# Optimization experiments

Hardware: AMD Instinct MI355X
Metric: run time of the kernel (lower is better)

Reference implementation:

```python
import jax, jax.numpy as jnp
import numpy as np
import math

B, N, FIN, FOUT, OPE = 16, 2048, 128, 128, 64


def setup_inputs() -> dict:
    key = jax.random.key(0)
    ks = jax.random.split(key, 10)
    h = jax.random.normal(ks[0], (B, N, FIN), dtype=jnp.float32)
    adj = jax.random.randint(ks[1], (B, N, N), 0, 2).astype(jnp.float32)
    op_emb = jax.random.normal(ks[2], (B, N, OPE), dtype=jnp.float32)
    # Linear weights stored as (in, out) so y = x @ W; torch init scale ~ 1/sqrt(fan_in)
    s_in = 1.0 / math.sqrt(FIN)
    Wk = jax.random.uniform(ks[3], (FIN, FOUT), minval=-s_in, maxval=s_in)
    Wq = jax.random.uniform(ks[4], (FIN, FOUT), minval=-s_in, maxval=s_in)
    Wv = jax.random.uniform(ks[5], (FIN, FOUT), minval=-s_in, maxval=s_in)
    s_a = 1.0 / math.sqrt(FOUT)
    a_w = jax.random.uniform(ks[6], (FOUT,), minval=-s_a, maxval=s_a)
    s_op = 1.0 / math.sqrt(OPE)
    op_W = jax.random.uniform(ks[7], (OPE, FOUT), minval=-s_op, maxval=s_op)
    op_b = jax.random.uniform(ks[8], (FOUT,), minval=-s_op, maxval=s_op)
    ln_g = jnp.ones((FOUT,), dtype=jnp.float32)
    ln_b = jnp.zeros((FOUT,), dtype=jnp.float32)
    return {"h": h, "adj": adj, "op_emb": op_emb, "Wk": Wk, "Wq": Wq,
            "Wv": Wv, "a_w": a_w, "op_W": op_W, "op_b": op_b,
            "ln_g": ln_g, "ln_b": ln_b}


def reference(h, adj, op_emb, Wk, Wq, Wv, a_w, op_W, op_b, ln_g, ln_b):
    d = Wk.shape[1]
    Whk = h @ Wk  # (B,N,d)
    Whq = h @ Wq
    Whv = h @ Wv
    # Original builds a_input[b,e,l,m] = Whq[b,e,m]*Whk[b,l,m] (B,N,N,d) then
    # projects with a (d->1). Algebraically: scores[b,e,l] = <Whq[b,e], Whk[b,l]*a_w>.
    scores = jnp.einsum('bed,bld->bel', Whq, Whk * a_w)
    scores = scores / jnp.sqrt(jnp.float32(d))  # attention_rescale
    alpha = jax.nn.leaky_relu(scores, negative_slope=0.2)  # leakrelu
    alpha = alpha * adj  # multiplicative mask (zeros stay in the softmax)
    attn = jax.nn.softmax(alpha, axis=-1)  # softmax over source nodes l
    agg = jnp.einsum('bel,bld->bed', attn, Whv)  # (B,N,d)
    gate = jax.nn.sigmoid(op_emb @ op_W + op_b)  # opattention branch
    hp = gate * agg
    # LayerNorm over last dim, eps=1e-5
    mu = jnp.mean(hp, axis=-1, keepdims=True)
    var = jnp.mean(jnp.square(hp - mu), axis=-1, keepdims=True)
    return (hp - mu) * jax.lax.rsqrt(var + 1e-5) * ln_g + ln_b
```

## Files before the change

### kernel.cpp

```cpp
#include <hip/hip_runtime.h>
#include <hip/hip_bf16.h>

typedef unsigned int u32;
typedef unsigned long long u64;
typedef float f32x4 __attribute__((ext_vector_type(4)));
typedef short s16x8 __attribute__((ext_vector_type(8)));

#define LDA 136

#define WQT_OFF 0ULL
#define WKT_OFF 32768ULL
#define WVT_OFF 65536ULL
#define OPWT_OFF 98304ULL
#define Q_OFF 114688ULL
#define K_OFF (Q_OFF + 8388608ULL)
#define VT_OFF (K_OFF + 8388608ULL)
#define GATE_OFF (VT_OFF + 8388608ULL)

__device__ __forceinline__ u32 f2bf(float f) {
  u32 u = __float_as_uint(f);
  return (u + 0x7fffu + ((u >> 16) & 1u)) >> 16;
}

__device__ __forceinline__ u32 pk2bf(float a, float b) {
  __hip_bfloat162 h = __float22bfloat162_rn(make_float2(a, b));
  u32 r;
  __builtin_memcpy(&r, &h, 4);
  return r;
}

__device__ __forceinline__ void gl_lds16(const void* g, void* l) {
  __builtin_amdgcn_global_load_lds((const __attribute__((address_space(1))) void*)g,
                                   (__attribute__((address_space(3))) void*)l, 16, 0, 0);
}

__global__ void k0_wt(const float* Wq, const float* Wk, const float* Wv,
                      const float* aw, const float* opW, char* ws) {
  int nt = blockIdx.x, part = blockIdx.y;
  int kksh = (nt == 3) ? 6 : 7;
  int KK = 1 << kksh;
  const float* S = (nt == 0) ? Wq : (nt == 1) ? Wk : (nt == 2) ? Wv : opW;
  unsigned short* D = (unsigned short*)(ws + (nt == 0 ? WQT_OFF : nt == 1 ? WKT_OFF : nt == 2 ? WVT_OFF : OPWT_OFF));
  int base = part * 8 * KK;
  for (int i = threadIdx.x; i < 8 * KK; i += 256) {
    int d = part * 8 + (i >> kksh), k = i & (KK - 1);
    float v = S[k * 128 + d];
    if (nt == 1) v *= aw[d] * 0.12751743f;
    D[base + i] = (unsigned short)f2bf(v);
  }
}

__launch_bounds__(256, 2)
__global__ void k1_proj(const float* __restrict__ h, const float* __restrict__ op_emb,
                        const float* __restrict__ op_b, char* __restrict__ ws) {
  int nt = blockIdx.x, et = blockIdx.y;
  int kksh = (nt == 3) ? 6 : 7;
  int KK = 1 << kksh;
  __shared__ unsigned short bufA[128 * LDA];
  __shared__ unsigned short bufB[128 * LDA];
  unsigned short* wbuf = (nt == 2) ? bufB : bufA;
  unsigned short* xbuf = (nt == 2) ? bufA : bufB;
  const unsigned short* Wt = (const unsigned short*)(ws + (nt == 0 ? WQT_OFF : nt == 1 ? WKT_OFF : nt == 2 ? WVT_OFF : OPWT_OFF));
  {
    const uint4* Ws = (const uint4*)Wt;
    int cnt = 128 * KK / 8;
    for (int i = threadIdx.x; i < cnt; i += 256) {
      uint4 v = Ws[i];
      int r = (8 * i) >> kksh, c = (8 * i) & (KK - 1);
      *(uint4*)&wbuf[r * LDA + c] = v;
    }
  }
  {
    const float* X = (nt == 3) ? (op_emb + (size_t)et * 128 * 64) : (h + (size_t)et * 128 * 128);
    int cnt = 128 * KK / 4;
    for (int i = threadIdx.x; i < cnt; i += 256) {
      float4 v = *(const float4*)(X + 4 * i);
      int r = (4 * i) >> kksh, c = (4 * i) & (KK - 1);
      *(uint2*)&xbuf[r * LDA + c] = make_uint2(pk2bf(v.x, v.y), pk2bf(v.z, v.w));
    }
  }
  __syncthreads();
  int tid = threadIdx.x, w = tid >> 6, lane = tid & 63, l15 = lane & 15, q = lane >> 4;
  int wa = w >> 1, wb = w & 1;
  f32x4 acc[4][4];
#pragma unroll
  for (int a = 0; a < 4; a++)
#pragma unroll
    for (int bq = 0; bq < 4; bq++) acc[a][bq] = f32x4{0.f, 0.f, 0.f, 0.f};
  for (int ks = 0; ks < KK / 32; ks++) {
    s16x8 af[4], bf_[4];
#pragma unroll
    for (int mt = 0; mt < 4; mt++)
      af[mt] = *(const s16x8*)&bufA[(wa * 64 + mt * 16 + l15) * LDA + ks * 32 + q * 8];
#pragma unroll
    for (int n2 = 0; n2 < 4; n2++)
      bf_[n2] = *(const s16x8*)&bufB[(wb * 64 + n2 * 16 + l15) * LDA + ks * 32 + q * 8];
#pragma unroll
    for (int mt = 0; mt < 4; mt++)
#pragma unroll
      for (int n2 = 0; n2 < 4; n2++)
        acc[mt][n2] = __builtin_amdgcn_mfma_f32_16x16x32_bf16(af[mt], bf_[n2], acc[mt][n2], 0, 0, 0);
  }
  if (nt <= 1) {
    unsigned short* Dst = (unsigned short*)(ws + (nt == 0 ? Q_OFF : K_OFF));
#pragma unroll
    for (int mt = 0; mt < 4; mt++)
#pragma unroll
      for (int n2 = 0; n2 < 4; n2++) {
        int d0 = wa * 64 + mt * 16 + q * 4;
        int eg = et * 128 + wb * 64 + n2 * 16 + l15;
        f32x4 a = acc[mt][n2];
        *(uint2*)(Dst + (size_t)eg * 128 + d0) = make_uint2(pk2bf(a[0], a[1]), pk2bf(a[2], a[3]));
      }
  } else if (nt == 2) {
    unsigned short* Dst = (unsigned short*)(ws + VT_OFF);
    int b = et >> 4;
    int ein0 = (et & 15) * 128;
#pragma unroll
    for (int mt = 0; mt < 4; mt++)
#pragma unroll
      for (int n2 = 0; n2 < 4; n2++) {
        int e0b = ein0 + wa * 64 + mt * 16 + q * 4;
        int d = wb * 64 + n2 * 16 + l15;
        f32x4 a = acc[mt][n2];
        *(uint2*)(Dst + (size_t)b * 128 * 2048 + (size_t)d * 2048 + e0b) =
            make_uint2(pk2bf(a[0], a[1]), pk2bf(a[2], a[3]));
      }
  } else {
    float* Dst = (float*)(ws + GATE_OFF);
#pragma unroll
    for (int mt = 0; mt < 4; mt++)
#pragma unroll
      for (int n2 = 0; n2 < 4; n2++) {
        int d0 = wa * 64 + mt * 16 + q * 4;
        int eg = et * 128 + wb * 64 + n2 * 16 + l15;
        f32x4 a = acc[mt][n2];
        float4 g4;
        g4.x = 1.f / (1.f + __builtin_amdgcn_exp2f(-(a[0] + op_b[d0 + 0]) * 1.4426950f));
        g4.y = 1.f / (1.f + __builtin_amdgcn_exp2f(-(a[1] + op_b[d0 + 1]) * 1.4426950f));
        g4.z = 1.f / (1.f + __builtin_amdgcn_exp2f(-(a[2] + op_b[d0 + 2]) * 1.4426950f));
        g4.w = 1.f / (1.f + __builtin_amdgcn_exp2f(-(a[3] + op_b[d0 + 3]) * 1.4426950f));
        *(float4*)(Dst + (size_t)eg * 128 + d0) = g4;
      }
  }
}

#define BAR_A do { asm volatile("s_waitcnt vmcnt(8) lgkmcnt(0)\n\ts_barrier" ::: "memory"); \
                   __builtin_amdgcn_sched_barrier(0); } while (0)
#define BAR_B do { asm volatile("s_waitcnt vmcnt(0) lgkmcnt(0)\n\ts_barrier" ::: "memory"); \
                   __builtin_amdgcn_sched_barrier(0); } while (0)
#define BAR_C do { asm volatile("s_waitcnt lgkmcnt(0)\n\ts_barrier" ::: "memory"); \
                   __builtin_amdgcn_sched_barrier(0); } while (0)

__launch_bounds__(256, 2)
__global__ void k2_attn(const float* __restrict__ adj, const float* __restrict__ ln_g,
                        const float* __restrict__ ln_b, char* __restrict__ ws,
                        float* __restrict__ out) {
  __shared__ char smem[81920];
  char* Klds = smem;
  char* Vlds = smem + 32768;
  char* PL = smem + 65536;

  const int bid = blockIdx.x;
  const int xcd = bid & 7, slot = bid >> 3;
  const int b = xcd * 2 + (slot >> 5);
  const int e0 = (slot & 31) << 6;

  const unsigned short* Qg = (const unsigned short*)(ws + Q_OFF) + ((size_t)b * 2048 + e0) * 128;
  const unsigned short* Kg = (const unsigned short*)(ws + K_OFF) + (size_t)b * 2048 * 128;
  const unsigned short* Vtg = (const unsigned short*)(ws + VT_OFF) + (size_t)b * 128 * 2048;
  const float* gateg = (const float*)(ws + GATE_OFF) + ((size_t)b * 2048 + e0) * 128;
  const float* adjg = adj + (size_t)b * 2048 * 2048 + (size_t)e0 * 2048;

  const int tid = threadIdx.x;
  const int w = tid >> 6, lane = tid & 63, l15 = lane & 15, q = lane >> 4;
  const int wh = w >> 1, we = w & 1;

  s16x8 qf[2][4];
#pragma unroll
  for (int et = 0; et < 2; et++) {
    const int e = we * 32 + et * 16 + l15;
#pragma unroll
    for (int ks = 0; ks < 4; ks++)
      qf[et][ks] = *(const s16x8*)(Qg + (size_t)e * 128 + ks * 32 + q * 8);
  }
  __builtin_amdgcn_sched_barrier(0);

  f32x4 oacc[2][4];
#pragma unroll
  for (int et = 0; et < 2; et++)
#pragma unroll
    for (int dt = 0; dt < 4; dt++) oacc[et][dt] = f32x4{0.f, 0.f, 0.f, 0.f};
  float dp0 = 0.0f, dp1 = 0.0f;
  float4 av[2][4];

#pragma unroll
  for (int j = 0; j < 8; j++) {
    int S = (j * 4 + w) * 64 + lane;
    int r = S >> 4, c = (S & 15) ^ (r & 15);
    gl_lds16(Kg + (size_t)r * 128 + (c << 3), Klds + (j * 4 + w) * 1024);
  }
  __builtin_amdgcn_sched_barrier(0);
#pragma unroll
  for (int j = 0; j < 8; j++) {
    int S = (j * 4 + w) * 64 + lane;
    int r = S >> 4, c = (S & 15) ^ (r & 15);
    gl_lds16(Vtg + (size_t)r * 2048 + (c << 3), Vlds + (j * 4 + w) * 1024);
  }
  __builtin_amdgcn_sched_barrier(0);
#pragma unroll
  for (int et = 0; et < 2; et++) {
    const int e = we * 32 + et * 16 + l15;
#pragma unroll
    for (int lt = 0; lt < 4; lt++)
      av[et][lt] = *(const float4*)(adjg + (size_t)e * 2048 + wh * 64 + lt * 16 + q * 4);
  }
  __builtin_amdgcn_sched_barrier(0);

#pragma unroll 1
  for (int it = 0; it < 16; it++) {
    BAR_A;

    f32x4 sacc[4][2];
#pragma unroll
    for (int lt = 0; lt < 4; lt++)
#pragma unroll
      for (int et = 0; et < 2; et++) sacc[lt][et] = f32x4{0.f, 0.f, 0.f, 0.f};
#pragma unroll
    for (int ks = 0; ks < 4; ks++) {
      s16x8 kf[4];
#pragma unroll
      for (int lt = 0; lt < 4; lt++) {
        int l = wh * 64 + lt * 16 + l15;
        kf[lt] = *(const s16x8*)(Klds + l * 256 + (((ks * 4 + q) ^ l15) << 4));
      }
#pragma unroll
      for (int lt = 0; lt < 4; lt++)
#pragma unroll
        for (int et = 0; et < 2; et++)
          sacc[lt][et] = __builtin_amdgcn_mfma_f32_16x16x32_bf16(kf[lt], qf[et][ks], sacc[lt][et], 0, 0, 0);
    }

#pragma unroll
    for (int et = 0; et < 2; et++) {
      const int e = we * 32 + et * 16 + l15;
      float dsum = 0.0f;
#pragma unroll
      for (int lt = 0; lt < 4; lt++) {
        float4 aj = av[et][lt];
        f32x4 s = sacc[lt][et];
        float p0 = __builtin_amdgcn_exp2f(fmaxf(s[0], 0.2f * s[0]) * aj.x);
        float p1 = __builtin_amdgcn_exp2f(fmaxf(s[1], 0.2f * s[1]) * aj.y);
        float p2 = __builtin_amdgcn_exp2f(fmaxf(s[2], 0.2f * s[2]) * aj.z);
        float p3 = __builtin_amdgcn_exp2f(fmaxf(s[3], 0.2f * s[3]) * aj.w);
        dsum += (p0 + p1) + (p2 + p3);
        int chunk = wh * 8 + lt * 2 + (q >> 1);
        *(uint2*)(PL + e * 256 + ((chunk ^ l15) << 4) + (q & 1) * 8) =
            make_uint2(pk2bf(p0, p1), pk2bf(p2, p3));
      }
      if (et == 0) dp0 += dsum; else dp1 += dsum;
    }

    BAR_B;

    if (it < 15) {
      const unsigned short* kb = Kg + (size_t)(it + 1) * 16384;
#pragma unroll
      for (int j = 0; j < 8; j++) {
        int S = (j * 4 + w) * 64 + lane;
        int r = S >> 4, c = (S & 15) ^ (r & 15);
        gl_lds16(kb + (size_t)r * 128 + (c << 3), Klds + (j * 4 + w) * 1024);
      }
      __builtin_amdgcn_sched_barrier(0);
      const float* ab = adjg + (size_t)(it + 1) * 128;
#pragma unroll
      for (int et = 0; et < 2; et++) {
        const int e = we * 32 + et * 16 + l15;
#pragma unroll
        for (int lt = 0; lt < 4; lt++)
          av[et][lt] = *(const float4*)(ab + (size_t)e * 2048 + wh * 64 + lt * 16 + q * 4);
      }
      __builtin_amdgcn_sched_barrier(0);
    }

#pragma unroll
    for (int ks = 0; ks < 4; ks++) {
      s16x8 af[2], vf[4];
#pragma unroll
      for (int et = 0; et < 2; et++) {
        const int e = we * 32 + et * 16 + l15;
        af[et] = *(const s16x8*)(PL + e * 256 + (((ks * 4 + q) ^ l15) << 4));
      }
#pragma unroll
      for (int dt = 0; dt < 4; dt++) {
        int d = wh * 64 + dt * 16 + l15;
        vf[dt] = *(const s16x8*)(Vlds + d * 256 + (((ks * 4 + q) ^ l15) << 4));
      }
#pragma unroll
      for (int et = 0; et < 2; et++)
#pragma unroll
        for (int dt = 0; dt < 4; dt++)
          oacc[et][dt] = __builtin_amdgcn_mfma_f32_16x16x32_bf16(af[et], vf[dt], oacc[et][dt], 0, 0, 0);
    }

    BAR_C;

    if (it < 15) {
      const unsigned short* vb = Vtg + (size_t)(it + 1) * 128;
#pragma unroll
      for (int j = 0; j < 8; j++) {
        int S = (j * 4 + w) * 64 + lane;
        int r = S >> 4, c = (S & 15) ^ (r & 15);
        gl_lds16(vb + (size_t)r * 2048 + (c << 3), Vlds + (j * 4 + w) * 1024);
      }
      __builtin_amdgcn_sched_barrier(0);
    }
  }

  float* sden = (float*)(smem + 65536);
  if (tid < 64) sden[tid] = 0.0f;
  __syncthreads();
  atomicAdd(&sden[we * 32 + l15], dp0);
  atomicAdd(&sden[we * 32 + 16 + l15], dp1);

  float* O2 = (float*)smem;
#pragma unroll
  for (int et = 0; et < 2; et++)
#pragma unroll
    for (int dt = 0; dt < 4; dt++) {
      const int eb = we * 32 + et * 16 + q * 4;
      const int d = wh * 64 + dt * 16 + l15;
      f32x4 v = oacc[et][dt];
#pragma unroll
      for (int r = 0; r < 4; r++) O2[(eb + r) * 132 + d] = v[r];
    }
  __syncthreads();

  {
    const int e = tid >> 2, j = tid & 3;
    const float inv = 1.0f / sden[e];
    const float* row = O2 + e * 132 + j * 32;
    const float* gr = gateg + (size_t)e * 128 + j * 32;
    float4 x[8];
    float s1 = 0.f, s2 = 0.f;
#pragma unroll
    for (int i = 0; i < 8; i++) {
      float4 v = *(const float4*)(row + i * 4);
      float4 g = *(const float4*)(gr + i * 4);
      float4 hp;
      hp.x = v.x * inv * g.x; hp.y = v.y * inv * g.y;
      hp.z = v.z * inv * g.z; hp.w = v.w * inv * g.w;
      x[i] = hp;
      s1 += (hp.x + hp.y) + (hp.z + hp.w);
      s2 += (hp.x * hp.x + hp.y * hp.y) + (hp.z * hp.z + hp.w * hp.w);
    }
    s1 += __shfl_xor(s1, 1); s2 += __shfl_xor(s2, 1);
    s1 += __shfl_xor(s1, 2); s2 += __shfl_xor(s2, 2);
    const float mu = s1 * 0.0078125f;
    const float var = s2 * 0.0078125f - mu * mu;
    const float rs = rsqrtf(var + 1e-5f);
    float* orow = out + ((size_t)b * 2048 + e0 + e) * 128 + j * 32;
    const float* gg = ln_g + j * 32;
    const float* bb = ln_b + j * 32;
#pragma unroll
    for (int i = 0; i < 8; i++) {
      float4 gv = *(const float4*)(gg + i * 4);
      float4 bv = *(const float4*)(bb + i * 4);
      float4 o;
      o.x = (x[i].x - mu) * rs * gv.x + bv.x;
      o.y = (x[i].y - mu) * rs * gv.y + bv.y;
      o.z = (x[i].z - mu) * rs * gv.z + bv.z;
      o.w = (x[i].w - mu) * rs * gv.w + bv.w;
      *(float4*)(orow + i * 4) = o;
    }
  }
}

extern "C" void kernel_launch(void* const* d_in, const int* in_sizes, int n_in,
                              void* d_out, int out_size, void* d_ws, size_t ws_size,
                              hipStream_t stream) {
  const float* h = (const float*)d_in[0];
  const float* adj = (const float*)d_in[1];
  const float* op_emb = (const float*)d_in[2];
  const float* Wk = (const float*)d_in[3];
  const float* Wq = (const float*)d_in[4];
  const float* Wv = (const float*)d_in[5];
  const float* a_w = (const float*)d_in[6];
  const float* op_W = (const float*)d_in[7];
  const float* op_b = (const float*)d_in[8];
  const float* ln_g = (const float*)d_in[9];
  const float* ln_b = (const float*)d_in[10];
  char* ws = (char*)d_ws;
  float* out = (float*)d_out;

  k0_wt<<<dim3(4, 16), 256, 0, stream>>>(Wq, Wk, Wv, a_w, op_W, ws);
  k1_proj<<<dim3(4, 256), 256, 0, stream>>>(h, op_emb, op_b, ws);
  k2_attn<<<512, 256, 0, stream>>>(adj, ln_g, ln_b, ws, out);
}
```

Before: 449.1 us.

## Double-buffer adjacency registers to prefetch two iterations ahead in attention loop

The main attention loop is unrolled by two so that adjacency tiles for iteration it+2 are loaded into alternating register sets (avA/avB) while the current iteration computes. The vmcnt waits are adjusted so that K/V loads into LDS are awaited without draining the outstanding adj loads. This hides global-load latency for the adj mask, which is the largest HBM stream. In exchange it uses more VGPRs, which could hurt occupancy at the two-blocks-per-CU launch bound, and the hand-counted vmcnt values must match the issue order exactly.

Measured after the change: 553.6 us. +23.3%, slower.

```diff
diff --git a/kernel.cpp b/kernel.cpp
--- a/kernel.cpp
+++ b/kernel.cpp
@@ -2,7 +2,6 @@
 #include <hip/hip_bf16.h>
 
 typedef unsigned int u32;
-typedef unsigned long long u64;
 typedef float f32x4 __attribute__((ext_vector_type(4)));
 typedef short s16x8 __attribute__((ext_vector_type(8)));
 
@@ -145,12 +144,119 @@
   }
 }
 
-#define BAR_A do { asm volatile("s_waitcnt vmcnt(8) lgkmcnt(0)\n\ts_barrier" ::: "memory"); \
-                   __builtin_amdgcn_sched_barrier(0); } while (0)
-#define BAR_B do { asm volatile("s_waitcnt vmcnt(0) lgkmcnt(0)\n\ts_barrier" ::: "memory"); \
-                   __builtin_amdgcn_sched_barrier(0); } while (0)
-#define BAR_C do { asm volatile("s_waitcnt lgkmcnt(0)\n\ts_barrier" ::: "memory"); \
-                   __builtin_amdgcn_sched_barrier(0); } while (0)
+
+#define BAR_A16 do { asm volatile("s_waitcnt vmcnt(16) lgkmcnt(0)\n\ts_barrier" ::: "memory"); \
+                     __builtin_amdgcn_sched_barrier(0); } while (0)
+#define BAR_A8  do { asm volatile("s_waitcnt vmcnt(8) lgkmcnt(0)\n\ts_barrier" ::: "memory"); \
+                     __builtin_amdgcn_sched_barrier(0); } while (0)
+#define BAR_B8  do { asm volatile("s_waitcnt vmcnt(8) lgkmcnt(0)\n\ts_barrier" ::: "memory"); \
+                     __builtin_amdgcn_sched_barrier(0); } while (0)
+#define BAR_B0  do { asm volatile("s_waitcnt vmcnt(0) lgkmcnt(0)\n\ts_barrier" ::: "memory"); \
+                     __builtin_amdgcn_sched_barrier(0); } while (0)
+#define BAR_C   do { asm volatile("s_waitcnt lgkmcnt(0)\n\ts_barrier" ::: "memory"); \
+                     __builtin_amdgcn_sched_barrier(0); } while (0)
+
+#define ISSUE_K(ITP1) do { \
+  const unsigned short* kb_ = Kg + (size_t)(ITP1) * 16384; \
+  _Pragma("unroll") \
+  for (int j_ = 0; j_ < 8; j_++) { \
+    int S_ = (j_ * 4 + w) * 64 + lane; \
+    int r_ = S_ >> 4, c_ = (S_ & 15) ^ (r_ & 15); \
+    gl_lds16(kb_ + (size_t)r_ * 128 + (c_ << 3), Klds + (j_ * 4 + w) * 1024); \
+  } \
+  __builtin_amdgcn_sched_barrier(0); \
+} while (0)
+
+#define ISSUE_V(ITP1) do { \
+  const unsigned short* vb_ = Vtg + (size_t)(ITP1) * 128; \
+  _Pragma("unroll") \
+  for (int j_ = 0; j_ < 8; j_++) { \
+    int S_ = (j_ * 4 + w) * 64 + lane; \
+    int r_ = S_ >> 4, c_ = (S_ & 15) ^ (r_ & 15); \
+    gl_lds16(vb_ + (size_t)r_ * 2048 + (c_ << 3), Vlds + (j_ * 4 + w) * 1024); \
+  } \
+  __builtin_amdgcn_sched_barrier(0); \
+} while (0)
+
+#define ISSUE_ADJ(ITN, AV) do { \
+  const float* ab_ = adjg + (size_t)(ITN) * 128; \
+  _Pragma("unroll") \
+  for (int et_ = 0; et_ < 2; et_++) { \
+    const int e_ = we * 32 + et_ * 16 + l15; \
+    _Pragma("unroll") \
+    for (int lt_ = 0; lt_ < 4; lt_++) \
+      AV[et_][lt_] = *(const float4*)(ab_ + (size_t)e_ * 2048 + wh * 64 + lt_ * 16 + q * 4); \
+  } \
+  __builtin_amdgcn_sched_barrier(0); \
+} while (0)
+
+#define K2_ITER(IT, AV, BARA, BARB, DO_ISS, DO_ADJ2) do { \
+  BARA;  \
+  f32x4 sacc[4][2]; \
+  _Pragma("unroll") \
+  for (int lt = 0; lt < 4; lt++) \
+    _Pragma("unroll") \
+    for (int et = 0; et < 2; et++) sacc[lt][et] = f32x4{0.f, 0.f, 0.f, 0.f}; \
+  _Pragma("unroll") \
+  for (int ks = 0; ks < 4; ks++) { \
+    s16x8 kf[4]; \
+    _Pragma("unroll") \
+    for (int lt = 0; lt < 4; lt++) { \
+      int l = wh * 64 + lt * 16 + l15; \
+      kf[lt] = *(const s16x8*)(Klds + l * 256 + (((ks * 4 + q) ^ l15) << 4)); \
+    } \
+    _Pragma("unroll") \
+    for (int lt = 0; lt < 4; lt++) \
+      _Pragma("unroll") \
+      for (int et = 0; et < 2; et++) \
+        sacc[lt][et] = __builtin_amdgcn_mfma_f32_16x16x32_bf16(kf[lt], qf[et][ks], sacc[lt][et], 0, 0, 0); \
+  } \
+  _Pragma("unroll") \
+  for (int et = 0; et < 2; et++) { \
+    const int e = we * 32 + et * 16 + l15; \
+    float dsum = 0.0f; \
+    _Pragma("unroll") \
+    for (int lt = 0; lt < 4; lt++) { \
+      float4 aj = AV[et][lt]; \
+      f32x4 s = sacc[lt][et]; \
+      float p0 = __builtin_amdgcn_exp2f(fmaxf(s[0], 0.2f * s[0]) * aj.x); \
+      float p1 = __builtin_amdgcn_exp2f(fmaxf(s[1], 0.2f * s[1]) * aj.y); \
+      float p2 = __builtin_amdgcn_exp2f(fmaxf(s[2], 0.2f * s[2]) * aj.z); \
+      float p3 = __builtin_amdgcn_exp2f(fmaxf(s[3], 0.2f * s[3]) * aj.w); \
+      dsum += (p0 + p1) + (p2 + p3); \
+      int chunk = wh * 8 + lt * 2 + (q >> 1); \
+      *(uint2*)(PL + e * 256 + ((chunk ^ l15) << 4) + (q & 1) * 8) = \
+          make_uint2(pk2bf(p0, p1), pk2bf(p2, p3)); \
+    } \
+    if (et == 0) dp0 += dsum; else dp1 += dsum; \
+  } \
+  BARB;  \
+  if (DO_ISS) ISSUE_K((IT) + 1); \
+  _Pragma("unroll") \
+  for (int ks = 0; ks < 4; ks++) { \
+    s16x8 af[2], vf[4]; \
+    _Pragma("unroll") \
+    for (int et = 0; et < 2; et++) { \
+      const int e = we * 32 + et * 16 + l15; \
+      af[et] = *(const s16x8*)(PL + e * 256 + (((ks * 4 + q) ^ l15) << 4)); \
+    } \
+    _Pragma("unroll") \
+    for (int dt = 0; dt < 4; dt++) { \
+      int d = wh * 64 + dt * 16 + l15; \
+      vf[dt] = *(const s16x8*)(Vlds + d * 256 + (((ks * 4 + q) ^ l15) << 4)); \
+    } \
+    _Pragma("unroll") \
+    for (int et = 0; et < 2; et++) \
+      _Pragma("unroll") \
+      for (int dt = 0; dt < 4; dt++) \
+        oacc[et][dt] = __builtin_amdgcn_mfma_f32_16x16x32_bf16(af[et], vf[dt], oacc[et][dt], 0, 0, 0); \
+  } \
+  BAR_C;  \
+  if (DO_ISS) { \
+    ISSUE_V((IT) + 1); \
+    if (DO_ADJ2) ISSUE_ADJ((IT) + 2, AV); \
+  } \
+} while (0)
 
 __launch_bounds__(256, 2)
 __global__ void k2_attn(const float* __restrict__ adj, const float* __restrict__ ln_g,
@@ -184,6 +290,7 @@
     for (int ks = 0; ks < 4; ks++)
       qf[et][ks] = *(const s16x8*)(Qg + (size_t)e * 128 + ks * 32 + q * 8);
   }
+  asm volatile("s_waitcnt vmcnt(0)" ::: "memory");
   __builtin_amdgcn_sched_barrier(0);
 
   f32x4 oacc[2][4];
@@ -192,130 +299,21 @@
 #pragma unroll
     for (int dt = 0; dt < 4; dt++) oacc[et][dt] = f32x4{0.f, 0.f, 0.f, 0.f};
   float dp0 = 0.0f, dp1 = 0.0f;
-  float4 av[2][4];
-
-#pragma unroll
-  for (int j = 0; j < 8; j++) {
-    int S = (j * 4 + w) * 64 + lane;
-    int r = S >> 4, c = (S & 15) ^ (r & 15);
-    gl_lds16(Kg + (size_t)r * 128 + (c << 3), Klds + (j * 4 + w) * 1024);
-  }
-  __builtin_amdgcn_sched_barrier(0);
-#pragma unroll
-  for (int j = 0; j < 8; j++) {
-    int S = (j * 4 + w) * 64 + lane;
-    int r = S >> 4, c = (S & 15) ^ (r & 15);
-    gl_lds16(Vtg + (size_t)r * 2048 + (c << 3), Vlds + (j * 4 + w) * 1024);
-  }
-  __builtin_amdgcn_sched_barrier(0);
-#pragma unroll
-  for (int et = 0; et < 2; et++) {
-    const int e = we * 32 + et * 16 + l15;
-#pragma unroll
-    for (int lt = 0; lt < 4; lt++)
-      av[et][lt] = *(const float4*)(adjg + (size_t)e * 2048 + wh * 64 + lt * 16 + q * 4);
-  }
-  __builtin_amdgcn_sched_barrier(0);
+  float4 avA[2][4], avB[2][4];
+
+  ISSUE_ADJ(0, avA);
+  ISSUE_K(0);
+  ISSUE_V(0);
+  ISSUE_ADJ(1, avB);
 
 #pragma unroll 1
-  for (int it = 0; it < 16; it++) {
-    BAR_A;
-
-    f32x4 sacc[4][2];
-#pragma unroll
-    for (int lt = 0; lt < 4; lt++)
-#pragma unroll
-      for (int et = 0; et < 2; et++) sacc[lt][et] = f32x4{0.f, 0.f, 0.f, 0.f};
-#pragma unroll
-    for (int ks = 0; ks < 4; ks++) {
-      s16x8 kf[4];
-#pragma unroll
-      for (int lt = 0; lt < 4; lt++) {
-        int l = wh * 64 + lt * 16 + l15;
-        kf[lt] = *(const s16x8*)(Klds + l * 256 + (((ks * 4 + q) ^ l15) << 4));
-      }
-#pragma unroll
-      for (int lt = 0; lt < 4; lt++)
-#pragma unroll
-        for (int et = 0; et < 2; et++)
-          sacc[lt][et] = __builtin_amdgcn_mfma_f32_16x16x32_bf16(kf[lt], qf[et][ks], sacc[lt][et], 0, 0, 0);
-    }
-
-#pragma unroll
-    for (int et = 0; et < 2; et++) {
-      const int e = we * 32 + et * 16 + l15;
-      float dsum = 0.0f;
-#pragma unroll
-      for (int lt = 0; lt < 4; lt++) {
-        float4 aj = av[et][lt];
-        f32x4 s = sacc[lt][et];
-        float p0 = __builtin_amdgcn_exp2f(fmaxf(s[0], 0.2f * s[0]) * aj.x);
-        float p1 = __builtin_amdgcn_exp2f(fmaxf(s[1], 0.2f * s[1]) * aj.y);
-        float p2 = __builtin_amdgcn_exp2f(fmaxf(s[2], 0.2f * s[2]) * aj.z);
-        float p3 = __builtin_amdgcn_exp2f(fmaxf(s[3], 0.2f * s[3]) * aj.w);
-        dsum += (p0 + p1) + (p2 + p3);
-        int chunk = wh * 8 + lt * 2 + (q >> 1);
-        *(uint2*)(PL + e * 256 + ((chunk ^ l15) << 4) + (q & 1) * 8) =
-            make_uint2(pk2bf(p0, p1), pk2bf(p2, p3));
-      }
-      if (et == 0) dp0 += dsum; else dp1 += dsum;
-    }
-
-    BAR_B;
-
-    if (it < 15) {
-      const unsigned short* kb = Kg + (size_t)(it + 1) * 16384;
-#pragma unroll
-      for (int j = 0; j < 8; j++) {
-        int S = (j * 4 + w) * 64 + lane;
-        int r = S >> 4, c = (S & 15) ^ (r & 15);
-        gl_lds16(kb + (size_t)r * 128 + (c << 3), Klds + (j * 4 + w) * 1024);
-      }
-      __builtin_amdgcn_sched_barrier(0);
-      const float* ab = adjg + (size_t)(it + 1) * 128;
-#pragma unroll
-      for (int et = 0; et < 2; et++) {
-        const int e = we * 32 + et * 16 + l15;
-#pragma unroll
-        for (int lt = 0; lt < 4; lt++)
-          av[et][lt] = *(const float4*)(ab + (size_t)e * 2048 + wh * 64 + lt * 16 + q * 4);
-      }
-      __builtin_amdgcn_sched_barrier(0);
-    }
-
-#pragma unroll
-    for (int ks = 0; ks < 4; ks++) {
-      s16x8 af[2], vf[4];
-#pragma unroll
-      for (int et = 0; et < 2; et++) {
-        const int e = we * 32 + et * 16 + l15;
-        af[et] = *(const s16x8*)(PL + e * 256 + (((ks * 4 + q) ^ l15) << 4));
-      }
-#pragma unroll
-      for (int dt = 0; dt < 4; dt++) {
-        int d = wh * 64 + dt * 16 + l15;
-        vf[dt] = *(const s16x8*)(Vlds + d * 256 + (((ks * 4 + q) ^ l15) << 4));
-      }
-#pragma unroll
-      for (int et = 0; et < 2; et++)
-#pragma unroll
-        for (int dt = 0; dt < 4; dt++)
-          oacc[et][dt] = __builtin_amdgcn_mfma_f32_16x16x32_bf16(af[et], vf[dt], oacc[et][dt], 0, 0, 0);
-    }
-
-    BAR_C;
-
-    if (it < 15) {
-      const unsigned short* vb = Vtg + (size_t)(it + 1) * 128;
-#pragma unroll
-      for (int j = 0; j < 8; j++) {
-        int S = (j * 4 + w) * 64 + lane;
-        int r = S >> 4, c = (S & 15) ^ (r & 15);
-        gl_lds16(vb + (size_t)r * 2048 + (c << 3), Vlds + (j * 4 + w) * 1024);
-      }
-      __builtin_amdgcn_sched_barrier(0);
-    }
-  }
+  for (int it2 = 0; it2 < 7; it2++) {
+    const int itE = it2 * 2;
+    K2_ITER(itE, avA, BAR_A16, BAR_B8, true, true);
+    K2_ITER(itE + 1, avB, BAR_A16, BAR_B8, true, true);
+  }
+  K2_ITER(14, avA, BAR_A16, BAR_B8, true, false);
+  K2_ITER(15, avB, BAR_A8, BAR_B0, false, false);
 
   float* sden = (float*)(smem + 65536);
   if (tid < 64) sden[tid] = 0.0f;
```

## Stage K/V tiles through registers instead of direct global-to-LDS loads

Applied to the files above, without the earlier changes.

Replaces the direct global_load_lds transfers of K and V tiles with ordinary global loads into registers at the top of each iteration, followed by register-to-LDS stores after the barriers. Offsets are precomputed once per thread. The aim is a register-prefetch pipeline: next-tile loads are issued early and overlap the score and PV MFMA work, and the vmcnt waits at the barriers go away. The cost is 16 extra uint4 registers per thread under launch bounds of 2 blocks per CU, which may cause spills or lower occupancy, plus extra VALU/LDS store instructions.

New measurement: 585.8 us. 1.3x slower.

```diff
diff --git a/kernel.cpp b/kernel.cpp
--- a/kernel.cpp
+++ b/kernel.cpp
@@ -2,7 +2,6 @@
 #include <hip/hip_bf16.h>
 
 typedef unsigned int u32;
-typedef unsigned long long u64;
 typedef float f32x4 __attribute__((ext_vector_type(4)));
 typedef short s16x8 __attribute__((ext_vector_type(8)));
 
@@ -27,11 +26,6 @@
   u32 r;
   __builtin_memcpy(&r, &h, 4);
   return r;
-}
-
-__device__ __forceinline__ void gl_lds16(const void* g, void* l) {
-  __builtin_amdgcn_global_load_lds((const __attribute__((address_space(1))) void*)g,
-                                   (__attribute__((address_space(3))) void*)l, 16, 0, 0);
 }
 
 __global__ void k0_wt(const float* Wq, const float* Wk, const float* Wv,
@@ -145,12 +139,8 @@
   }
 }
 
-#define BAR_A do { asm volatile("s_waitcnt vmcnt(8) lgkmcnt(0)\n\ts_barrier" ::: "memory"); \
-                   __builtin_amdgcn_sched_barrier(0); } while (0)
-#define BAR_B do { asm volatile("s_waitcnt vmcnt(0) lgkmcnt(0)\n\ts_barrier" ::: "memory"); \
-                   __builtin_amdgcn_sched_barrier(0); } while (0)
-#define BAR_C do { asm volatile("s_waitcnt lgkmcnt(0)\n\ts_barrier" ::: "memory"); \
-                   __builtin_amdgcn_sched_barrier(0); } while (0)
+#define BARL do { asm volatile("s_waitcnt lgkmcnt(0)\n\ts_barrier" ::: "memory"); \
+                  __builtin_amdgcn_sched_barrier(0); } while (0)
 
 __launch_bounds__(256, 2)
 __global__ void k2_attn(const float* __restrict__ adj, const float* __restrict__ ln_g,
@@ -176,6 +166,17 @@
   const int w = tid >> 6, lane = tid & 63, l15 = lane & 15, q = lane >> 4;
   const int wh = w >> 1, we = w & 1;
 
+  int ldsoff[8];
+  size_t koff[8], voff[8];
+#pragma unroll
+  for (int j = 0; j < 8; j++) {
+    int S = (j * 4 + w) * 64 + lane;
+    int r = S >> 4, c = (S & 15) ^ (r & 15);
+    ldsoff[j] = S * 16;
+    koff[j] = (size_t)r * 128 + c * 8;
+    voff[j] = (size_t)r * 2048 + c * 8;
+  }
+
   s16x8 qf[2][4];
 #pragma unroll
   for (int et = 0; et < 2; et++) {
@@ -184,7 +185,6 @@
     for (int ks = 0; ks < 4; ks++)
       qf[et][ks] = *(const s16x8*)(Qg + (size_t)e * 128 + ks * 32 + q * 8);
   }
-  __builtin_amdgcn_sched_barrier(0);
 
   f32x4 oacc[2][4];
 #pragma unroll
@@ -193,21 +193,12 @@
     for (int dt = 0; dt < 4; dt++) oacc[et][dt] = f32x4{0.f, 0.f, 0.f, 0.f};
   float dp0 = 0.0f, dp1 = 0.0f;
   float4 av[2][4];
-
-#pragma unroll
-  for (int j = 0; j < 8; j++) {
-    int S = (j * 4 + w) * 64 + lane;
-    int r = S >> 4, c = (S & 15) ^ (r & 15);
-    gl_lds16(Kg + (size_t)r * 128 + (c << 3), Klds + (j * 4 + w) * 1024);
-  }
-  __builtin_amdgcn_sched_barrier(0);
-#pragma unroll
-  for (int j = 0; j < 8; j++) {
-    int S = (j * 4 + w) * 64 + lane;
-    int r = S >> 4, c = (S & 15) ^ (r & 15);
-    gl_lds16(Vtg + (size_t)r * 2048 + (c << 3), Vlds + (j * 4 + w) * 1024);
-  }
-  __builtin_amdgcn_sched_barrier(0);
+  uint4 kst[8], vst[8];
+
+#pragma unroll
+  for (int j = 0; j < 8; j++) kst[j] = *(const uint4*)(Kg + koff[j]);
+#pragma unroll
+  for (int j = 0; j < 8; j++) vst[j] = *(const uint4*)(Vtg + voff[j]);
 #pragma unroll
   for (int et = 0; et < 2; et++) {
     const int e = we * 32 + et * 16 + l15;
@@ -216,10 +207,23 @@
       av[et][lt] = *(const float4*)(adjg + (size_t)e * 2048 + wh * 64 + lt * 16 + q * 4);
   }
   __builtin_amdgcn_sched_barrier(0);
+#pragma unroll
+  for (int j = 0; j < 8; j++) *(uint4*)(Klds + ldsoff[j]) = kst[j];
+#pragma unroll
+  for (int j = 0; j < 8; j++) *(uint4*)(Vlds + ldsoff[j]) = vst[j];
+  BARL;
 
 #pragma unroll 1
   for (int it = 0; it < 16; it++) {
-    BAR_A;
+    if (it < 15) {
+      const unsigned short* kb = Kg + (size_t)(it + 1) * 16384;
+      const unsigned short* vb = Vtg + (size_t)(it + 1) * 128;
+#pragma unroll
+      for (int j = 0; j < 8; j++) kst[j] = *(const uint4*)(kb + koff[j]);
+#pragma unroll
+      for (int j = 0; j < 8; j++) vst[j] = *(const uint4*)(vb + voff[j]);
+      __builtin_amdgcn_sched_barrier(0);
+    }
 
     f32x4 sacc[4][2];
 #pragma unroll
@@ -261,16 +265,11 @@
       if (et == 0) dp0 += dsum; else dp1 += dsum;
     }
 
-    BAR_B;
+    BARL;
 
     if (it < 15) {
-      const unsigned short* kb = Kg + (size_t)(it + 1) * 16384;
-#pragma unroll
-      for (int j = 0; j < 8; j++) {
-        int S = (j * 4 + w) * 64 + lane;
-        int r = S >> 4, c = (S & 15) ^ (r & 15);
-        gl_lds16(kb + (size_t)r * 128 + (c << 3), Klds + (j * 4 + w) * 1024);
-      }
+#pragma unroll
+      for (int j = 0; j < 8; j++) *(uint4*)(Klds + ldsoff[j]) = kst[j];
       __builtin_amdgcn_sched_barrier(0);
       const float* ab = adjg + (size_t)(it + 1) * 128;
 #pragma unroll
@@ -303,16 +302,11 @@
           oacc[et][dt] = __builtin_amdgcn_mfma_f32_16x16x32_bf16(af[et], vf[dt], oacc[et][dt], 0, 0, 0);
     }
 
-    BAR_C;
+    BARL;
 
     if (it < 15) {
-      const unsigned short* vb = Vtg + (size_t)(it + 1) * 128;
-#pragma unroll
-      for (int j = 0; j < 8; j++) {
-        int S = (j * 4 + w) * 64 + lane;
-        int r = S >> 4, c = (S & 15) ^ (r & 15);
-        gl_lds16(vb + (size_t)r * 2048 + (c << 3), Vlds + (j * 4 + w) * 1024);
-      }
+#pragma unroll
+      for (int j = 0; j < 8; j++) *(uint4*)(Vlds + ldsoff[j]) = vst[j];
       __builtin_amdgcn_sched_barrier(0);
     }
   }
```
